# Performance work log

Hardware: AMD Instinct MI355X
Metric: run time of the kernel (lower is better)

## Reference

```python
import jax, jax.numpy as jnp
import numpy as np

MUL = 64          # multiplicity of every irrep block
EMB = 64

# --- normalize_function(gelu): scale phi so E[phi(N(0,1))^2] = 1 (e3nn convention) ---
_z = np.linspace(-8.0, 8.0, 4001)
_gauss = np.exp(-0.5 * _z**2) / np.sqrt(2.0 * np.pi)
_PHI_C = float(np.sqrt(np.trapz(np.asarray(jax.nn.gelu(jnp.asarray(_z)))**2 * _gauss, _z)))

# Levi-Civita tensor (real Wigner 3j for 1x1->1 up to normalization)
_eps = np.zeros((3, 3, 3), np.float32)
for (i, j, k), s in {(0,1,2):1,(1,2,0):1,(2,0,1):1,(0,2,1):-1,(2,1,0):-1,(1,0,2):-1}.items():
    _eps[i, j, k] = s
EPS = jnp.asarray(_eps)

INV_SQ3 = 1.0 / np.sqrt(3.0)   # w3j(1,1,0) component (after sqrt(2l3+1) component-norm scaling)
INV_SQ2 = 1.0 / np.sqrt(2.0)   # eps/sqrt(6) * sqrt(3)
ALPHA_01 = 1.0 / np.sqrt(2.0 * MUL * MUL)  # two uvw paths feed outputs 0e and 1o
ALPHA_2  = 1.0 / np.sqrt(1.0 * MUL * MUL)  # one path feeds 1e


def _mlp(x, Ws):
    # haiku Linear(no bias, N(0,1) init), x -> phi(x @ W / sqrt(fan_in)) with normalized phi
    for W in Ws:
        x = jax.nn.gelu(x @ W * (x.shape[-1] ** -0.5)) / _PHI_C
    return x


def setup_inputs() -> dict:
    key = jax.random.key(0)
    ks = jax.random.split(key, 11)
    B = 128
    return {
        "emb": jax.random.normal(ks[0], (B, EMB), jnp.float32),
        "x1": jax.random.normal(ks[1], (B, 4 * MUL), jnp.float32),   # 64x0e + 64x1o
        "x2": jax.random.normal(ks[2], (B, 4 * MUL), jnp.float32),
        "W0": jax.random.normal(ks[3], (EMB, 256), jnp.float32),
        "W1": jax.random.normal(ks[4], (256, 256), jnp.float32),
        "W2": jax.random.normal(ks[5], (256, 64), jnp.float32),
        "P0": jax.random.normal(ks[6], (64, MUL, MUL, MUL), jnp.float32),
        "P1": jax.random.normal(ks[7], (64, MUL, MUL, MUL), jnp.float32),
        "P2": jax.random.normal(ks[8], (64, MUL, MUL, MUL), jnp.float32),
        "P3": jax.random.normal(ks[9], (64, MUL, MUL, MUL), jnp.float32),
        "P4": jax.random.normal(ks[10], (64, MUL, MUL, MUL), jnp.float32),
    }


def reference(emb, x1, x2, W0, W1, W2, P0, P1, P2, P3, P4):
    B = emb.shape[0]
    # MLP -> per-sample weight vector h  [B, 64]
    h = _mlp(emb, (W0, W1, W2))
    hs = h * (h.shape[-1] ** -0.5)  # / sqrt(w.shape[0])
    # per-instruction generated path weights  [B, u, v, w]
    w0, w1, w2, w3, w4 = (jnp.einsum('xuvw,bx->buvw', P, hs) for P in (P0, P1, P2, P3, P4))

    s1, v1 = x1[:, :MUL], x1[:, MUL:].reshape(B, MUL, 3)
    s2, v2 = x2[:, :MUL], x2[:, MUL:].reshape(B, MUL, 3)

    # (0e,0e)->0e and (1o,1o)->0e
    t0 = jnp.einsum('bu,bv,buvw->bw', s1, s2, w0)
    t3 = jnp.einsum('bui,bvi,buvw->bw', v1, v2, w3) * INV_SQ3
    out0 = ALPHA_01 * (t0 + t3)                      # [B, MUL]
    # (0e,1o)->1o and (1o,0e)->1o
    t1 = jnp.einsum('bu,bvj,buvw->bwj', s1, v2, w1)
    t2 = jnp.einsum('bui,bv,buvw->bwi', v1, s2, w2)
    out1 = ALPHA_01 * (t1 + t2)                      # [B, MUL, 3]
    # (1o,1o)->1e  (cross-product path)
    t4 = jnp.einsum('bui,bvj,buvw,ijk->bwk', v1, v2, w4, EPS) * INV_SQ2
    out2 = ALPHA_2 * t4                              # [B, MUL, 3]

    return jnp.concatenate([out0, out1.reshape(B, 3 * MUL), out2.reshape(B, 3 * MUL)], axis=-1)
```

## Files before the change

### kernel.cpp

```cpp
#include <hip/hip_runtime.h>

typedef float v4f __attribute__((ext_vector_type(4)));
typedef short v8s __attribute__((ext_vector_type(8)));

__device__ __forceinline__ unsigned short f2bf_rn(float f) {
  unsigned u = __float_as_uint(f);
  return (unsigned short)((u + 0x7fffu + ((u >> 16) & 1u)) >> 16);
}
__device__ __forceinline__ float bf2f(unsigned short h) {
  return __uint_as_float((unsigned)h << 16);
}

__device__ __forceinline__ float gelu_phi(float x) {
  float t = tanhf(0.7978845608f * (x + 0.044715f * x * x * x));
  return 0.5f * x * (1.0f + t) * 1.5338375f;
}

__global__ __launch_bounds__(256) void k_mlp1(const float* __restrict__ emb, const float* __restrict__ W0,
                                              const float* __restrict__ x1, const float* __restrict__ x2,
                                              float* __restrict__ act1,
                                              unsigned short* __restrict__ s1c, unsigned short* __restrict__ v1c,
                                              unsigned short* __restrict__ s2c, unsigned short* __restrict__ v2c)
{
  const int blk = blockIdx.x, tid = threadIdx.x;
  if (blk < 128) {
    float s = 0.f;
#pragma unroll 8
    for (int xx = 0; xx < 64; ++xx) s += emb[blk * 64 + xx] * W0[xx * 256 + tid];
    act1[blk * 256 + tid] = gelu_phi(s * 0.125f);
  } else {
    const int sel = (blk - 128) >> 3;
    const float* xs = sel ? x2 : x1;
    unsigned short* sc = sel ? s2c : s1c;
    unsigned short* vc = sel ? v2c : v1c;
    for (int i = ((blk - 128) & 7) * 256 + tid; i < 32768; i += 2048) {
      if (i < 8192) {
        sc[i] = f2bf_rn(xs[(i >> 6) * 256 + (i & 63)]);
      } else {
        const int t = i - 8192, g = t >> 13, r = t & 8191;
        vc[g * 8192 + r] = f2bf_rn(xs[(r >> 6) * 256 + 64 + (r & 63) * 3 + g]);
      }
    }
  }
}

__global__ __launch_bounds__(256) void k_mlp2(const float* __restrict__ act1, const float* __restrict__ W1,
                                              float* __restrict__ act2)
{
  const int b = blockIdx.x, j = threadIdx.x;
  float s = 0.f;
#pragma unroll 16
  for (int x = 0; x < 256; ++x) s += act1[b * 256 + x] * W1[x * 256 + j];
  act2[b * 256 + j] = gelu_phi(s * 0.0625f);
}

__global__ __launch_bounds__(256) void k_mlp3(const float* __restrict__ act2, const float* __restrict__ W2,
                                              float* __restrict__ hsT)
{
  const int o = blockIdx.x * 256 + threadIdx.x;
  const int b = o >> 6, e = o & 63;
  float s = 0.f;
#pragma unroll 16
  for (int x = 0; x < 256; ++x) s += act2[b * 256 + x] * W2[x * 64 + e];
  hsT[e * 128 + b] = gelu_phi(s * 0.0625f) * 0.125f;
}


template<int G>
__device__ __forceinline__ void gemm_body(
    const float* __restrict__ P,
    const unsigned short* __restrict__ f1g,
    const unsigned short* __restrict__ f2g,
    const float* __restrict__ hsT,
    float* __restrict__ partial,
    int c, int csh,
    unsigned short* ldsF1, unsigned* ldsB32)
{
  constexpr int NC  = (G == 0 || G == 3) ? 1 : 3;
  constexpr int NF2 = (G == 0 || G == 2) ? 1 : 3;
  constexpr int NH  = (G == 0 || G == 1) ? 1 : 3;
  constexpr int NCM = (G <= 1) ? 1 : 3;
  constexpr int RB  = (G == 0) ? 0 : (G == 1) ? 128 : (G == 2) ? 512 : (G == 3) ? 896 : 1024;

  const int tid = threadIdx.x;
  const int lane = tid & 63, w = tid >> 6, l16 = lane & 15, quad = lane >> 4;
  const int tq = tid & 15, kp = tid >> 4;
  const int x = c >> (csh - 6);
  const int nsub = 1 << (7 - csh);

  int bidx[2];
  bidx[0] = w * 32 + l16;
  bidx[1] = w * 32 + 16 + l16;

  float hsx[2];
  hsx[0] = hsT[x * 128 + bidx[0]];
  hsx[1] = hsT[x * 128 + bidx[1]];

  v8s fr2[2][NF2][2];
#pragma unroll
  for (int bh = 0; bh < 2; ++bh)
#pragma unroll
    for (int m = 0; m < NF2; ++m)
#pragma unroll
      for (int h = 0; h < 2; ++h)
        fr2[bh][m][h] = *(const v8s*)(f2g + m * 8192 + bidx[bh] * 64 + h * 32 + quad * 8);

  v4f acc[2][NC][4];
#pragma unroll
  for (int bh = 0; bh < 2; ++bh)
#pragma unroll
    for (int cc = 0; cc < NC; ++cc)
#pragma unroll
      for (int nf = 0; nf < 4; ++nf) acc[bh][cc][nf] = (v4f){0.f, 0.f, 0.f, 0.f};

  const int swz_w = (tq & 3) << 2;
  const int swz_r = ((l16 >> 2) & 3) << 2;

  float h[2][NH];

  for (int sub = 0; sub < nsub; ++sub) {
    const int kb = (c << (18 - csh)) + (sub << 11);
    const int u0 = (kb >> 6) & 63;
    __syncthreads();
    {
      const int nchk = NCM * 512;
      for (int i = tid; i < nchk; i += 256) {
        const int uu8 = i & 3, b = (i >> 2) & 127, cm = i >> 9;
        *(v8s*)&ldsF1[(cm * 128 + b) * 40 + uu8 * 8] =
            *(const v8s*)(f1g + cm * 8192 + b * 64 + u0 + uu8 * 8);
      }
    }

    auto gload = [&](int kk, float4& r0, float4& r1) {
      const float* s = P + (size_t)(kb + kk * 32 + 2 * kp) * 64 + 4 * tq;
      r0 = *(const float4*)s;
      r1 = *(const float4*)(s + 64);
    };
    auto bwrite = [&](int buf, const float4& r0, const float4& r1) {
      unsigned* dst = ldsB32 + (size_t)(buf * 64 + 4 * tq) * 20 + (kp ^ swz_w);
      dst[0]  = (unsigned)f2bf_rn(r0.x) | ((unsigned)f2bf_rn(r1.x) << 16);
      dst[20] = (unsigned)f2bf_rn(r0.y) | ((unsigned)f2bf_rn(r1.y) << 16);
      dst[40] = (unsigned)f2bf_rn(r0.z) | ((unsigned)f2bf_rn(r1.z) << 16);
      dst[60] = (unsigned)f2bf_rn(r0.w) | ((unsigned)f2bf_rn(r1.w) << 16);
    };

    float4 pa0, pa1;
    gload(0, pa0, pa1);
    bwrite(0, pa0, pa1);
    gload(1, pa0, pa1);
    __syncthreads();

#pragma unroll 2
    for (int kk = 0; kk < 64; ++kk) {
      const int buf = kk & 1;
      const int vh = kk & 1;
      v8s bfr[4];
#pragma unroll
      for (int nf = 0; nf < 4; ++nf)
        bfr[nf] = *(const v8s*)&ldsB32[(size_t)(buf * 64 + nf * 16 + l16) * 20 + ((quad * 4) ^ swz_r)];
      if (vh == 0) {
        const int uu = kk >> 1;
#pragma unroll
        for (int bh = 0; bh < 2; ++bh)
#pragma unroll
          for (int m = 0; m < NH; ++m)
            h[bh][m] = hsx[bh] * bf2f(ldsF1[m * 5120 + bidx[bh] * 40 + uu]);
      }
      if (kk < 63) bwrite(buf ^ 1, pa0, pa1);
      if (kk < 62) gload(kk + 2, pa0, pa1);
#pragma unroll
      for (int bh = 0; bh < 2; ++bh) {
#pragma unroll
        for (int cc = 0; cc < NC; ++cc) {
          v8s af;
#pragma unroll
          for (int j = 0; j < 8; ++j) {
            float p;
            if constexpr (G == 0)
              p = h[bh][0] * bf2f((unsigned short)fr2[bh][0][vh][j]);
            else if constexpr (G == 1)
              p = h[bh][0] * bf2f((unsigned short)fr2[bh][cc][vh][j]);
            else if constexpr (G == 2)
              p = h[bh][cc] * bf2f((unsigned short)fr2[bh][0][vh][j]);
            else if constexpr (G == 3)
              p = h[bh][0] * bf2f((unsigned short)fr2[bh][0][vh][j])
                + h[bh][1] * bf2f((unsigned short)fr2[bh][1][vh][j])
                + h[bh][2] * bf2f((unsigned short)fr2[bh][2][vh][j]);
            else {
              const int i1 = (cc + 1) % 3, j2 = (cc + 2) % 3;
              p = h[bh][i1] * bf2f((unsigned short)fr2[bh][j2][vh][j])
                - h[bh][j2] * bf2f((unsigned short)fr2[bh][i1][vh][j]);
            }
            af[j] = (short)(__float_as_uint(p) >> 16);
          }
#pragma unroll
          for (int nf = 0; nf < 4; ++nf)
            acc[bh][cc][nf] = __builtin_amdgcn_mfma_f32_16x16x32_bf16(af, bfr[nf], acc[bh][cc][nf], 0, 0, 0);
        }
      }
      __syncthreads();
    }
  }

#pragma unroll
  for (int bh = 0; bh < 2; ++bh)
#pragma unroll
    for (int cc = 0; cc < NC; ++cc)
#pragma unroll
      for (int nf = 0; nf < 4; ++nf)
#pragma unroll
        for (int r = 0; r < 4; ++r) {
          const int row = RB + cc * 128 + w * 32 + bh * 16 + quad * 4 + r;
          partial[((size_t)c * 1408 + row) * 64 + nf * 16 + l16] = acc[bh][cc][nf][r];
        }
}

__global__ __launch_bounds__(256, 2) void tp_gemm(
    const float* __restrict__ P0, const float* __restrict__ P1, const float* __restrict__ P2,
    const float* __restrict__ P3, const float* __restrict__ P4,
    const unsigned short* __restrict__ s1c, const unsigned short* __restrict__ v1c,
    const unsigned short* __restrict__ s2c, const unsigned short* __restrict__ v2c,
    const float* __restrict__ hsT, float* __restrict__ partial, int csh)
{
  __shared__ __align__(16) unsigned ldsB32[2 * 64 * 20];
  __shared__ __align__(16) unsigned short ldsF1[3 * 128 * 40];
  const int g = blockIdx.x >> csh;
  const int c = blockIdx.x & ((1 << csh) - 1);
  switch (g) {
    case 0: gemm_body<0>(P0, s1c, s2c, hsT, partial, c, csh, ldsF1, ldsB32); break;
    case 1: gemm_body<1>(P1, s1c, v2c, hsT, partial, c, csh, ldsF1, ldsB32); break;
    case 2: gemm_body<2>(P2, v1c, s2c, hsT, partial, c, csh, ldsF1, ldsB32); break;
    case 3: gemm_body<3>(P3, v1c, v2c, hsT, partial, c, csh, ldsF1, ldsB32); break;
    default: gemm_body<4>(P4, v1c, v2c, hsT, partial, c, csh, ldsF1, ldsB32); break;
  }
}

__global__ __launch_bounds__(448) void k_fin(const float* __restrict__ partial, float* __restrict__ out, int nch)
{
  const int b = blockIdx.x, i = threadIdx.x;
  int w, rA, rB;
  if (i < 64)       { w = i; rA = b; rB = 896 + b; }
  else if (i < 256) { const int t = i - 64;  w = t / 3; const int j = t - 3 * w; rA = 128 + j * 128 + b; rB = 512 + j * 128 + b; }
  else              { const int t = i - 256; w = t / 3; const int k = t - 3 * w; rA = 1024 + k * 128 + b; rB = rA; }
  const float* pA = partial + (size_t)rA * 64 + w;
  const float* pB = partial + (size_t)rB * 64 + w;
  float sA = 0.f, sB = 0.f;
#pragma unroll 4
  for (int cc = 0; cc < nch; ++cc) {
    sA += pA[(size_t)cc * 90112];
    sB += pB[(size_t)cc * 90112];
  }
  const float A01 = 0.011048543f;
  const float sc = 0.015625f * 0.70710678f;
  float o;
  if (i < 64)       o = A01 * (sA + 0.57735027f * sB);
  else if (i < 256) o = A01 * (sA + sB);
  else              o = sc * sA;
  out[b * 448 + i] = o;
}

extern "C" void kernel_launch(void* const* d_in, const int* in_sizes, int n_in,
                              void* d_out, int out_size, void* d_ws, size_t ws_size,
                              hipStream_t stream)
{
  const float* emb = (const float*)d_in[0];
  const float* x1  = (const float*)d_in[1];
  const float* x2  = (const float*)d_in[2];
  const float* W0  = (const float*)d_in[3];
  const float* W1  = (const float*)d_in[4];
  const float* W2  = (const float*)d_in[5];
  const float* P0  = (const float*)d_in[6];
  const float* P1  = (const float*)d_in[7];
  const float* P2  = (const float*)d_in[8];
  const float* P3  = (const float*)d_in[9];
  const float* P4  = (const float*)d_in[10];
  float* out = (float*)d_out;
  char* ws = (char*)d_ws;

  float* hsT = (float*)ws;
  unsigned short* s1c = (unsigned short*)(ws + 32768);
  unsigned short* v1c = (unsigned short*)(ws + 49152);
  unsigned short* s2c = (unsigned short*)(ws + 98304);
  unsigned short* v2c = (unsigned short*)(ws + 114688);
  float* act1 = (float*)(ws + 163840);
  float* act2 = (float*)(ws + 294912);
  float* partial = (float*)(ws + 163840);

  const int csh = (ws_size >= (size_t)163840 + ((size_t)360448 << 7)) ? 7 : 6;

  k_mlp1<<<144, 256, 0, stream>>>(emb, W0, x1, x2, act1, s1c, v1c, s2c, v2c);
  k_mlp2<<<128, 256, 0, stream>>>(act1, W1, act2);
  k_mlp3<<<32, 256, 0, stream>>>(act2, W2, hsT);
  tp_gemm<<<5 << csh, 256, 0, stream>>>(P0, P1, P2, P3, P4, s1c, v1c, s2c, v2c, hsT, partial, csh);
  k_fin<<<128, 448, 0, stream>>>(partial, out, 1 << csh);
}
```

Before: 398.5 us.

## Fuse MLP kernels, use packed bf16 converts, relax barriers, refine LDS swizzle

The three MLP launches are merged into one kernel that keeps the per-sample activations in shared memory, which removes two launches and their global round trips. In the tensor-product GEMM, manual bf16 rounding is replaced by the hardware packed convert instruction for both the P tiles and the A fragments. __syncthreads is replaced by an lgkmcnt-only wait plus s_barrier so in-flight global prefetches are not drained at each step. The LDS swizzle now also XORs by the high tq bits and by nf, to reduce bank conflicts. Rounding behavior of the A fragments changes from truncation to round-to-nearest, and the barrier change depends on the compiler not reordering the global loads.

```diff
diff --git a/kernel.cpp b/kernel.cpp
--- a/kernel.cpp
+++ b/kernel.cpp
@@ -10,24 +10,64 @@
 __device__ __forceinline__ float bf2f(unsigned short h) {
   return __uint_as_float((unsigned)h << 16);
 }
+__device__ __forceinline__ unsigned cvt_pk_bf16(float lo, float hi) {
+  unsigned r;
+  asm("v_cvt_pk_bf16_f32 %0, %1, %2" : "=v"(r) : "v"(lo), "v"(hi));
+  return r;
+}
+
+__device__ __forceinline__ void barrier_keep_vmcnt() {
+  asm volatile("s_waitcnt lgkmcnt(0)" ::: "memory");
+  __builtin_amdgcn_s_barrier();
+}
 
 __device__ __forceinline__ float gelu_phi(float x) {
   float t = tanhf(0.7978845608f * (x + 0.044715f * x * x * x));
   return 0.5f * x * (1.0f + t) * 1.5338375f;
 }
 
-__global__ __launch_bounds__(256) void k_mlp1(const float* __restrict__ emb, const float* __restrict__ W0,
-                                              const float* __restrict__ x1, const float* __restrict__ x2,
-                                              float* __restrict__ act1,
-                                              unsigned short* __restrict__ s1c, unsigned short* __restrict__ v1c,
-                                              unsigned short* __restrict__ s2c, unsigned short* __restrict__ v2c)
+__global__ __launch_bounds__(256) void k_mlp(const float* __restrict__ emb, const float* __restrict__ W0,
+                                             const float* __restrict__ W1, const float* __restrict__ W2,
+                                             const float* __restrict__ x1, const float* __restrict__ x2,
+                                             float* __restrict__ hsT,
+                                             unsigned short* __restrict__ s1c, unsigned short* __restrict__ v1c,
+                                             unsigned short* __restrict__ s2c, unsigned short* __restrict__ v2c)
 {
   const int blk = blockIdx.x, tid = threadIdx.x;
   if (blk < 128) {
-    float s = 0.f;
+    __shared__ float er[64];
+    __shared__ float a1[256];
+    __shared__ float a2[256];
+    __shared__ float r3[4][64];
+    const int b = blk;
+    if (tid < 64) er[tid] = emb[b * 64 + tid];
+    __syncthreads();
+    {
+      float s = 0.f;
 #pragma unroll 8
-    for (int xx = 0; xx < 64; ++xx) s += emb[blk * 64 + xx] * W0[xx * 256 + tid];
-    act1[blk * 256 + tid] = gelu_phi(s * 0.125f);
+      for (int x = 0; x < 64; ++x) s += er[x] * W0[x * 256 + tid];
+      a1[tid] = gelu_phi(s * 0.125f);
+    }
+    __syncthreads();
+    {
+      float s = 0.f;
+#pragma unroll 16
+      for (int x = 0; x < 256; ++x) s += a1[x] * W1[x * 256 + tid];
+      a2[tid] = gelu_phi(s * 0.0625f);
+    }
+    __syncthreads();
+    {
+      const int e = tid & 63, q = tid >> 6;
+      float s = 0.f;
+#pragma unroll 16
+      for (int x = q * 64; x < q * 64 + 64; ++x) s += a2[x] * W2[x * 64 + e];
+      r3[q][e] = s;
+    }
+    __syncthreads();
+    if (tid < 64) {
+      const float s = r3[0][tid] + r3[1][tid] + r3[2][tid] + r3[3][tid];
+      hsT[tid * 128 + b] = gelu_phi(s * 0.0625f) * 0.125f;
+    }
   } else {
     const int sel = (blk - 128) >> 3;
     const float* xs = sel ? x2 : x1;
@@ -44,27 +84,6 @@
   }
 }
 
-__global__ __launch_bounds__(256) void k_mlp2(const float* __restrict__ act1, const float* __restrict__ W1,
-                                              float* __restrict__ act2)
-{
-  const int b = blockIdx.x, j = threadIdx.x;
-  float s = 0.f;
-#pragma unroll 16
-  for (int x = 0; x < 256; ++x) s += act1[b * 256 + x] * W1[x * 256 + j];
-  act2[b * 256 + j] = gelu_phi(s * 0.0625f);
-}
-
-__global__ __launch_bounds__(256) void k_mlp3(const float* __restrict__ act2, const float* __restrict__ W2,
-                                              float* __restrict__ hsT)
-{
-  const int o = blockIdx.x * 256 + threadIdx.x;
-  const int b = o >> 6, e = o & 63;
-  float s = 0.f;
-#pragma unroll 16
-  for (int x = 0; x < 256; ++x) s += act2[b * 256 + x] * W2[x * 64 + e];
-  hsT[e * 128 + b] = gelu_phi(s * 0.0625f) * 0.125f;
-}
-
 
 template<int G>
 __device__ __forceinline__ void gemm_body(
@@ -102,8 +121,8 @@
 #pragma unroll
     for (int m = 0; m < NF2; ++m)
 #pragma unroll
-      for (int h = 0; h < 2; ++h)
-        fr2[bh][m][h] = *(const v8s*)(f2g + m * 8192 + bidx[bh] * 64 + h * 32 + quad * 8);
+      for (int hh = 0; hh < 2; ++hh)
+        fr2[bh][m][hh] = *(const v8s*)(f2g + m * 8192 + bidx[bh] * 64 + hh * 32 + quad * 8);
 
   v4f acc[2][NC][4];
 #pragma unroll
@@ -113,8 +132,7 @@
 #pragma unroll
       for (int nf = 0; nf < 4; ++nf) acc[bh][cc][nf] = (v4f){0.f, 0.f, 0.f, 0.f};
 
-  const int swz_w = (tq & 3) << 2;
-  const int swz_r = ((l16 >> 2) & 3) << 2;
+  const int swz_w = (((tq & 3) ^ (tq >> 2)) << 2);
 
   float h[2][NH];
 
@@ -131,24 +149,24 @@
       }
     }
 
-    auto gload = [&](int kk, float4& r0, float4& r1) {
+    float4 pa0, pa1;
+    auto gload = [&](int kk) {
       const float* s = P + (size_t)(kb + kk * 32 + 2 * kp) * 64 + 4 * tq;
-      r0 = *(const float4*)s;
-      r1 = *(const float4*)(s + 64);
+      pa0 = *(const float4*)s;
+      pa1 = *(const float4*)(s + 64);
     };
-    auto bwrite = [&](int buf, const float4& r0, const float4& r1) {
-      unsigned* dst = ldsB32 + (size_t)(buf * 64 + 4 * tq) * 20 + (kp ^ swz_w);
-      dst[0]  = (unsigned)f2bf_rn(r0.x) | ((unsigned)f2bf_rn(r1.x) << 16);
-      dst[20] = (unsigned)f2bf_rn(r0.y) | ((unsigned)f2bf_rn(r1.y) << 16);
-      dst[40] = (unsigned)f2bf_rn(r0.z) | ((unsigned)f2bf_rn(r1.z) << 16);
-      dst[60] = (unsigned)f2bf_rn(r0.w) | ((unsigned)f2bf_rn(r1.w) << 16);
+    auto bwrite = [&](int buf) {
+      unsigned* dst = ldsB32 + (buf * 64 + 4 * tq) * 20 + (kp ^ swz_w);
+      dst[0]  = cvt_pk_bf16(pa0.x, pa1.x);
+      dst[20] = cvt_pk_bf16(pa0.y, pa1.y);
+      dst[40] = cvt_pk_bf16(pa0.z, pa1.z);
+      dst[60] = cvt_pk_bf16(pa0.w, pa1.w);
     };
 
-    float4 pa0, pa1;
-    gload(0, pa0, pa1);
-    bwrite(0, pa0, pa1);
-    gload(1, pa0, pa1);
-    __syncthreads();
+    gload(0);
+    bwrite(0);
+    gload(1);
+    barrier_keep_vmcnt();
 
 #pragma unroll 2
     for (int kk = 0; kk < 64; ++kk) {
@@ -157,7 +175,8 @@
       v8s bfr[4];
 #pragma unroll
       for (int nf = 0; nf < 4; ++nf)
-        bfr[nf] = *(const v8s*)&ldsB32[(size_t)(buf * 64 + nf * 16 + l16) * 20 + ((quad * 4) ^ swz_r)];
+        bfr[nf] = *(const v8s*)&ldsB32[(buf * 64 + nf * 16 + l16) * 20 +
+                                       ((quad * 4) ^ ((((l16 >> 2) & 3) ^ nf) << 2))];
       if (vh == 0) {
         const int uu = kk >> 1;
 #pragma unroll
@@ -166,39 +185,40 @@
           for (int m = 0; m < NH; ++m)
             h[bh][m] = hsx[bh] * bf2f(ldsF1[m * 5120 + bidx[bh] * 40 + uu]);
       }
-      if (kk < 63) bwrite(buf ^ 1, pa0, pa1);
-      if (kk < 62) gload(kk + 2, pa0, pa1);
+      if (kk < 63) bwrite(buf ^ 1);
+      if (kk < 62) gload(kk + 2);
 #pragma unroll
       for (int bh = 0; bh < 2; ++bh) {
 #pragma unroll
         for (int cc = 0; cc < NC; ++cc) {
-          v8s af;
-#pragma unroll
-          for (int j = 0; j < 8; ++j) {
-            float p;
+          auto pv = [&](int j) -> float {
             if constexpr (G == 0)
-              p = h[bh][0] * bf2f((unsigned short)fr2[bh][0][vh][j]);
+              return h[bh][0] * bf2f((unsigned short)(vh ? fr2[bh][0][1][j] : fr2[bh][0][0][j]));
             else if constexpr (G == 1)
-              p = h[bh][0] * bf2f((unsigned short)fr2[bh][cc][vh][j]);
+              return h[bh][0] * bf2f((unsigned short)(vh ? fr2[bh][cc][1][j] : fr2[bh][cc][0][j]));
             else if constexpr (G == 2)
-              p = h[bh][cc] * bf2f((unsigned short)fr2[bh][0][vh][j]);
+              return h[bh][cc] * bf2f((unsigned short)(vh ? fr2[bh][0][1][j] : fr2[bh][0][0][j]));
             else if constexpr (G == 3)
-              p = h[bh][0] * bf2f((unsigned short)fr2[bh][0][vh][j])
-                + h[bh][1] * bf2f((unsigned short)fr2[bh][1][vh][j])
-                + h[bh][2] * bf2f((unsigned short)fr2[bh][2][vh][j]);
+              return h[bh][0] * bf2f((unsigned short)(vh ? fr2[bh][0][1][j] : fr2[bh][0][0][j]))
+                   + h[bh][1] * bf2f((unsigned short)(vh ? fr2[bh][1][1][j] : fr2[bh][1][0][j]))
+                   + h[bh][2] * bf2f((unsigned short)(vh ? fr2[bh][2][1][j] : fr2[bh][2][0][j]));
             else {
               const int i1 = (cc + 1) % 3, j2 = (cc + 2) % 3;
-              p = h[bh][i1] * bf2f((unsigned short)fr2[bh][j2][vh][j])
-                - h[bh][j2] * bf2f((unsigned short)fr2[bh][i1][vh][j]);
+              return h[bh][i1] * bf2f((unsigned short)(vh ? fr2[bh][j2][1][j] : fr2[bh][j2][0][j]))
+                   - h[bh][j2] * bf2f((unsigned short)(vh ? fr2[bh][i1][1][j] : fr2[bh][i1][0][j]));
             }
-            af[j] = (short)(__float_as_uint(p) >> 16);
-          }
+          };
+          v8s af;
+          unsigned* a32 = (unsigned*)&af;
+#pragma unroll
+          for (int t = 0; t < 4; ++t)
+            a32[t] = cvt_pk_bf16(pv(2 * t), pv(2 * t + 1));
 #pragma unroll
           for (int nf = 0; nf < 4; ++nf)
             acc[bh][cc][nf] = __builtin_amdgcn_mfma_f32_16x16x32_bf16(af, bfr[nf], acc[bh][cc][nf], 0, 0, 0);
         }
       }
-      __syncthreads();
+      barrier_keep_vmcnt();
     }
   }
 
@@ -245,7 +265,7 @@
   const float* pA = partial + (size_t)rA * 64 + w;
   const float* pB = partial + (size_t)rB * 64 + w;
   float sA = 0.f, sB = 0.f;
-#pragma unroll 4
+#pragma unroll 8
   for (int cc = 0; cc < nch; ++cc) {
     sA += pA[(size_t)cc * 90112];
     sB += pB[(size_t)cc * 90112];
@@ -282,15 +302,11 @@
   unsigned short* v1c = (unsigned short*)(ws + 49152);
   unsigned short* s2c = (unsigned short*)(ws + 98304);
   unsigned short* v2c = (unsigned short*)(ws + 114688);
-  float* act1 = (float*)(ws + 163840);
-  float* act2 = (float*)(ws + 294912);
   float* partial = (float*)(ws + 163840);
 
   const int csh = (ws_size >= (size_t)163840 + ((size_t)360448 << 7)) ? 7 : 6;
 
-  k_mlp1<<<144, 256, 0, stream>>>(emb, W0, x1, x2, act1, s1c, v1c, s2c, v2c);
-  k_mlp2<<<128, 256, 0, stream>>>(act1, W1, act2);
-  k_mlp3<<<32, 256, 0, stream>>>(act2, W2, hsT);
+  k_mlp<<<144, 256, 0, stream>>>(emb, W0, W1, W2, x1, x2, hsT, s1c, v1c, s2c, v2c);
   tp_gemm<<<5 << csh, 256, 0, stream>>>(P0, P1, P2, P3, P4, s1c, v1c, s2c, v2c, hsT, partial, csh);
   k_fin<<<128, 448, 0, stream>>>(partial, out, 1 << csh);
 }
```

Result: slower. 497.0 us (+24.7%).
